# Kernel tuning notes

Hardware: AMD Instinct MI355X
Metric: run time of the kernel (lower is better)

Reference implementation:

```python
import jax, jax.numpy as jnp
import numpy as np

N = 100000
SAMPLE = 25
FEAT = 128
HIDDEN = 128
CLASSES = 40


def setup_inputs() -> dict:
    key = jax.random.key(0)
    k_x, k_n, k_w1, k_w2, k_wl = jax.random.split(key, 5)
    X = jax.random.normal(k_x, (N, FEAT), dtype=jnp.float32)
    neighbors = jax.random.randint(k_n, (N, SAMPLE), 0, N, dtype=jnp.int32)
    # torch Linear weights are [out_features, in_features], xavier-uniform init
    def xavier(k, out_d, in_d):
        bound = float(np.sqrt(6.0 / (in_d + out_d)))
        return jax.random.uniform(k, (out_d, in_d), dtype=jnp.float32, minval=-bound, maxval=bound)
    W1 = xavier(k_w1, HIDDEN, FEAT)
    W2 = xavier(k_w2, HIDDEN, HIDDEN)
    Wlast = xavier(k_wl, CLASSES, HIDDEN)
    return {"X": X, "neighbors": neighbors, "W1": W1, "W2": W2, "Wlast": Wlast}


def reference(X, neighbors, W1, W2, Wlast):
    # forward: for each layer W: X = spmm(adj, X); X = X @ W.T; relu(X)
    # adj row i has sample_num entries of value 1/sample_num -> mean over sampled neighbors
    h = X
    for W in (W1, W2):
        agg = jnp.mean(h[neighbors], axis=1)          # [N, sample, d] -> [N, d]
        h = jax.nn.relu(jnp.einsum('nd,hd->nh', agg, W))
    return jnp.einsum('nh,ch->nc', h, Wlast)          # [N, class_num]
```

## Files before the change

kernel.cpp:

```cpp
#include <hip/hip_runtime.h>
#include <cstdint>
#include <cstddef>

typedef unsigned short u16;
typedef __bf16 bf16x8 __attribute__((ext_vector_type(8)));
typedef u16 u16x8 __attribute__((ext_vector_type(8)));
typedef float f32x4 __attribute__((ext_vector_type(4)));

#define N_NODES 100000
#define SAMPLE 25
#define FEAT 128
#define CLASSES 40

__device__ __forceinline__ float bf2f(u16 v) {
    return __uint_as_float(((unsigned)v) << 16);
}
__device__ __forceinline__ u16 f2bf(float f) {
    unsigned u = __float_as_uint(f);
    u += 0x7FFFu + ((u >> 16) & 1u);
    return (u16)(u >> 16);
}
__device__ __forceinline__ void split_bf(float x, u16& hi, u16& lo) {
    hi = f2bf(x);
    lo = f2bf(x - bf2f(hi));
}

__device__ __forceinline__ void split8(const float* ap, bf16x8& ah, bf16x8& al) {
    union { u16x8 u; bf16x8 b; } H, L;
    #pragma unroll
    for (int j = 0; j < 8; ++j) {
        u16 h, lo; split_bf(ap[j], h, lo);
        H.u[j] = h; L.u[j] = lo;
    }
    ah = H.b; al = L.b;
}

__device__ __forceinline__ f32x4 mfma_split(bf16x8 ah, bf16x8 al,
                                            bf16x8 bh, bf16x8 bl, f32x4 acc) {
    acc = __builtin_amdgcn_mfma_f32_16x16x32_bf16(ah, bh, acc, 0, 0, 0);
    acc = __builtin_amdgcn_mfma_f32_16x16x32_bf16(al, bh, acc, 0, 0, 0);
    acc = __builtin_amdgcn_mfma_f32_16x16x32_bf16(ah, bl, acc, 0, 0, 0);
    return acc;
}

__global__ __launch_bounds__(256) void prep_weights(
    const float* __restrict__ W1, const float* __restrict__ W2,
    const float* __restrict__ Wl,
    u16* __restrict__ w1h, u16* __restrict__ w1l,
    u16* __restrict__ w2h, u16* __restrict__ w2l,
    u16* __restrict__ wlh, u16* __restrict__ wll)
{
    const int i = blockIdx.x * 256 + threadIdx.x;
    const int stride = gridDim.x * 256;
    for (int j = i; j < FEAT * FEAT; j += stride) {
        split_bf(W1[j], w1h[j], w1l[j]);
        split_bf(W2[j], w2h[j], w2l[j]);
    }
    for (int j = i; j < CLASSES * FEAT; j += stride) {
        split_bf(Wl[j], wlh[j], wll[j]);
    }
}

#define NPB32 32

__global__ __launch_bounds__(128) void k1_gemm(
    const float* __restrict__ X,
    const u16* __restrict__ w1h, const u16* __restrict__ w1l,
    u16* __restrict__ Z1)
{
    const int t = threadIdx.x;
    const int w  = t >> 6;
    const int l  = t & 63;
    const int lr = l & 15;
    const int lq = l >> 4;
    const int blockStart = blockIdx.x * NPB32;
    const float* Xrow = X + (size_t)(blockStart + w * 16 + lr) * FEAT;

    bf16x8 ah[4], al[4];
    #pragma unroll
    for (int k = 0; k < 4; ++k) {
        f32x4 x0 = *(const f32x4*)(Xrow + k * 32 + lq * 8);
        f32x4 x1 = *(const f32x4*)(Xrow + k * 32 + lq * 8 + 4);
        float tmp[8];
        #pragma unroll
        for (int j = 0; j < 4; ++j) { tmp[j] = x0[j]; tmp[4 + j] = x1[j]; }
        split8(tmp, ah[k], al[k]);
    }

    #pragma unroll
    for (int c = 0; c < 8; ++c) {
        f32x4 acc = {0.f, 0.f, 0.f, 0.f};
        #pragma unroll
        for (int k = 0; k < 4; ++k) {
            const size_t off = (size_t)(c * 16 + lr) * FEAT + k * 32 + lq * 8;
            bf16x8 bh = *(const bf16x8*)(w1h + off);
            bf16x8 bl = *(const bf16x8*)(w1l + off);
            acc = mfma_split(ah[k], al[k], bh, bl, acc);
        }
        #pragma unroll
        for (int r = 0; r < 4; ++r) {
            int node = blockStart + w * 16 + lq * 4 + r;
            Z1[(size_t)node * FEAT + c * 16 + lr] = f2bf(acc[r]);
        }
    }
}

__global__ __launch_bounds__(128) void k2_hop(
    const u16* __restrict__ Zin, const int* __restrict__ nb,
    const u16* __restrict__ wh, const u16* __restrict__ wl,
    u16* __restrict__ Zout)
{
    __shared__ int nbs[NPB32 * SAMPLE];
    __shared__ float agg[NPB32][FEAT + 4];

    const int t = threadIdx.x;
    const int blockStart = blockIdx.x * NPB32;

    for (int i = t; i < NPB32 * SAMPLE; i += 128)
        nbs[i] = nb[blockStart * SAMPLE + i];
    __syncthreads();

    for (int item = t; item < NPB32 * 16; item += 128) {
        const int nl = item >> 4;
        const int fg = item & 15;
        float acc[8];
        #pragma unroll
        for (int j = 0; j < 8; ++j) acc[j] = 0.f;
        const int* myn = &nbs[nl * SAMPLE];
        #pragma unroll 5
        for (int s = 0; s < SAMPLE; ++s) {
            u16x8 v = *(const u16x8*)(Zin + (size_t)myn[s] * FEAT + fg * 8);
            #pragma unroll
            for (int j = 0; j < 8; ++j) acc[j] += bf2f(v[j]);
        }
        #pragma unroll
        for (int j = 0; j < 8; ++j) {
            float m = acc[j] * (1.0f / SAMPLE);
            agg[nl][fg * 8 + j] = m > 0.f ? m : 0.f;
        }
    }
    __syncthreads();

    const int w  = t >> 6;
    const int l  = t & 63;
    const int lr = l & 15;
    const int lq = l >> 4;

    bf16x8 ah[4], al[4];
    #pragma unroll
    for (int k = 0; k < 4; ++k)
        split8(&agg[w * 16 + lr][k * 32 + lq * 8], ah[k], al[k]);

    #pragma unroll
    for (int c = 0; c < 8; ++c) {
        f32x4 acc = {0.f, 0.f, 0.f, 0.f};
        #pragma unroll
        for (int k = 0; k < 4; ++k) {
            const size_t off = (size_t)(c * 16 + lr) * FEAT + k * 32 + lq * 8;
            bf16x8 bh = *(const bf16x8*)(wh + off);
            bf16x8 bl = *(const bf16x8*)(wl + off);
            acc = mfma_split(ah[k], al[k], bh, bl, acc);
        }
        #pragma unroll
        for (int r = 0; r < 4; ++r) {
            int node = blockStart + w * 16 + lq * 4 + r;
            Zout[(size_t)node * FEAT + c * 16 + lr] = f2bf(acc[r]);
        }
    }
}

__global__ __launch_bounds__(128) void k3_hop(
    const u16* __restrict__ Zin, const int* __restrict__ nb,
    const u16* __restrict__ wh, const u16* __restrict__ wl,
    float* __restrict__ out)
{
    __shared__ int nbs[NPB32 * SAMPLE];
    __shared__ float agg[NPB32][FEAT + 4];

    const int t = threadIdx.x;
    const int blockStart = blockIdx.x * NPB32;

    for (int i = t; i < NPB32 * SAMPLE; i += 128)
        nbs[i] = nb[blockStart * SAMPLE + i];
    __syncthreads();

    for (int item = t; item < NPB32 * 16; item += 128) {
        const int nl = item >> 4;
        const int fg = item & 15;
        float acc[8];
        #pragma unroll
        for (int j = 0; j < 8; ++j) acc[j] = 0.f;
        const int* myn = &nbs[nl * SAMPLE];
        #pragma unroll 5
        for (int s = 0; s < SAMPLE; ++s) {
            u16x8 v = *(const u16x8*)(Zin + (size_t)myn[s] * FEAT + fg * 8);
            #pragma unroll
            for (int j = 0; j < 8; ++j) acc[j] += bf2f(v[j]);
        }
        #pragma unroll
        for (int j = 0; j < 8; ++j) {
            float m = acc[j] * (1.0f / SAMPLE);
            agg[nl][fg * 8 + j] = m > 0.f ? m : 0.f;
        }
    }
    __syncthreads();

    const int w  = t >> 6;
    const int l  = t & 63;
    const int lr = l & 15;
    const int lq = l >> 4;

    bf16x8 ah[4], al[4];
    #pragma unroll
    for (int k = 0; k < 4; ++k)
        split8(&agg[w * 16 + lr][k * 32 + lq * 8], ah[k], al[k]);

    #pragma unroll
    for (int c = 0; c < 3; ++c) {
        const int o = c * 16 + lr;
        f32x4 acc = {0.f, 0.f, 0.f, 0.f};
        #pragma unroll
        for (int k = 0; k < 4; ++k) {
            bf16x8 bh, bl;
            if (o < CLASSES) {
                const size_t off = (size_t)o * FEAT + k * 32 + lq * 8;
                bh = *(const bf16x8*)(wh + off);
                bl = *(const bf16x8*)(wl + off);
            } else {
                #pragma unroll
                for (int j = 0; j < 8; ++j) { bh[j] = (__bf16)0.f; bl[j] = (__bf16)0.f; }
            }
            acc = mfma_split(ah[k], al[k], bh, bl, acc);
        }
        if (o < CLASSES) {
            #pragma unroll
            for (int r = 0; r < 4; ++r) {
                int node = blockStart + w * 16 + lq * 4 + r;
                out[(size_t)node * CLASSES + o] = acc[r];
            }
        }
    }
}

#define NPB 64
#define AGG_STRIDE 136

__global__ __launch_bounds__(256) void gnn_layer1(
    const float* __restrict__ X, const int* __restrict__ nb,
    const u16* __restrict__ w1h, const u16* __restrict__ w1l,
    u16* __restrict__ h1)
{
    __shared__ int nbs[NPB * SAMPLE];
    __shared__ u16 agg_h[NPB][AGG_STRIDE];
    __shared__ u16 agg_l[NPB][AGG_STRIDE];

    const int t = threadIdx.x;
    const int blockStart = blockIdx.x * NPB;

    for (int i = t; i < NPB * SAMPLE; i += 256) {
        int gi = blockStart * SAMPLE + i;
        if (gi >= N_NODES * SAMPLE) gi = N_NODES * SAMPLE - 1;
        nbs[i] = nb[gi];
    }
    __syncthreads();

    for (int item = t; item < NPB * 16; item += 256) {
        const int nl = item >> 4;
        const int fg = item & 15;
        float acc[8];
        #pragma unroll
        for (int j = 0; j < 8; ++j) acc[j] = 0.f;
        const int* myn = &nbs[nl * SAMPLE];
        for (int s = 0; s < SAMPLE; ++s) {
            const float4* p = (const float4*)(X + (size_t)myn[s] * FEAT + fg * 8);
            float4 a = p[0], b = p[1];
            acc[0] += a.x; acc[1] += a.y; acc[2] += a.z; acc[3] += a.w;
            acc[4] += b.x; acc[5] += b.y; acc[6] += b.z; acc[7] += b.w;
        }
        u16x8 oh, ol;
        #pragma unroll
        for (int j = 0; j < 8; ++j) {
            float m = acc[j] * (1.0f / SAMPLE);
            u16 h, lo; split_bf(m, h, lo);
            oh[j] = h; ol[j] = lo;
        }
        *(u16x8*)&agg_h[nl][fg * 8] = oh;
        *(u16x8*)&agg_l[nl][fg * 8] = ol;
    }
    __syncthreads();

    const int w  = t >> 6;
    const int l  = t & 63;
    const int lr = l & 15;
    const int lq = l >> 4;

    bf16x8 ah[4], al[4];
    #pragma unroll
    for (int k = 0; k < 4; ++k) {
        ah[k] = *(const bf16x8*)&agg_h[w * 16 + lr][k * 32 + lq * 8];
        al[k] = *(const bf16x8*)&agg_l[w * 16 + lr][k * 32 + lq * 8];
    }

    #pragma unroll
    for (int c = 0; c < 8; ++c) {
        f32x4 acc = {0.f, 0.f, 0.f, 0.f};
        #pragma unroll
        for (int k = 0; k < 4; ++k) {
            const size_t off = (size_t)(c * 16 + lr) * FEAT + k * 32 + lq * 8;
            bf16x8 bh = *(const bf16x8*)(w1h + off);
            bf16x8 bl = *(const bf16x8*)(w1l + off);
            acc = mfma_split(ah[k], al[k], bh, bl, acc);
        }
        #pragma unroll
        for (int r = 0; r < 4; ++r) {
            int node = blockStart + w * 16 + lq * 4 + r;
            if (node < N_NODES) {
                float v = acc[r] > 0.f ? acc[r] : 0.f;
                h1[(size_t)node * FEAT + c * 16 + lr] = f2bf(v);
            }
        }
    }
}

__global__ __launch_bounds__(256) void gnn_layer2_final(
    const u16* __restrict__ h1, const int* __restrict__ nb,
    const u16* __restrict__ w2h, const u16* __restrict__ w2l,
    const u16* __restrict__ wlh, const u16* __restrict__ wll,
    float* __restrict__ out)
{
    __shared__ int nbs[NPB * SAMPLE];
    __shared__ u16 agg_h[NPB][AGG_STRIDE];
    __shared__ u16 agg_l[NPB][AGG_STRIDE];

    const int t = threadIdx.x;
    const int blockStart = blockIdx.x * NPB;

    for (int i = t; i < NPB * SAMPLE; i += 256) {
        int gi = blockStart * SAMPLE + i;
        if (gi >= N_NODES * SAMPLE) gi = N_NODES * SAMPLE - 1;
        nbs[i] = nb[gi];
    }
    __syncthreads();

    for (int item = t; item < NPB * 16; item += 256) {
        const int nl = item >> 4;
        const int fg = item & 15;
        float acc[8];
        #pragma unroll
        for (int j = 0; j < 8; ++j) acc[j] = 0.f;
        const int* myn = &nbs[nl * SAMPLE];
        for (int s = 0; s < SAMPLE; ++s) {
            u16x8 v = *(const u16x8*)(h1 + (size_t)myn[s] * FEAT + fg * 8);
            #pragma unroll
            for (int j = 0; j < 8; ++j) acc[j] += bf2f(v[j]);
        }
        u16x8 oh, ol;
        #pragma unroll
        for (int j = 0; j < 8; ++j) {
            float m = acc[j] * (1.0f / SAMPLE);
            u16 h, lo; split_bf(m, h, lo);
            oh[j] = h; ol[j] = lo;
        }
        *(u16x8*)&agg_h[nl][fg * 8] = oh;
        *(u16x8*)&agg_l[nl][fg * 8] = ol;
    }
    __syncthreads();

    const int w  = t >> 6;
    const int l  = t & 63;
    const int lr = l & 15;
    const int lq = l >> 4;

    f32x4 hacc[8];
    {
        bf16x8 ah[4], al[4];
        #pragma unroll
        for (int k = 0; k < 4; ++k) {
            ah[k] = *(const bf16x8*)&agg_h[w * 16 + lr][k * 32 + lq * 8];
            al[k] = *(const bf16x8*)&agg_l[w * 16 + lr][k * 32 + lq * 8];
        }
        #pragma unroll
        for (int c = 0; c < 8; ++c) {
            f32x4 acc = {0.f, 0.f, 0.f, 0.f};
            #pragma unroll
            for (int k = 0; k < 4; ++k) {
                const size_t off = (size_t)(c * 16 + lr) * FEAT + k * 32 + lq * 8;
                bf16x8 bh = *(const bf16x8*)(w2h + off);
                bf16x8 bl = *(const bf16x8*)(w2l + off);
                acc = mfma_split(ah[k], al[k], bh, bl, acc);
            }
            hacc[c] = acc;
        }
    }
    __syncthreads();

    #pragma unroll
    for (int c = 0; c < 8; ++c) {
        #pragma unroll
        for (int r = 0; r < 4; ++r) {
            float v = hacc[c][r] > 0.f ? hacc[c][r] : 0.f;
            u16 h, l2; split_bf(v, h, l2);
            agg_h[w * 16 + lq * 4 + r][c * 16 + lr] = h;
            agg_l[w * 16 + lq * 4 + r][c * 16 + lr] = l2;
        }
    }
    __syncthreads();

    {
        bf16x8 ah[4], al[4];
        #pragma unroll
        for (int k = 0; k < 4; ++k) {
            ah[k] = *(const bf16x8*)&agg_h[w * 16 + lr][k * 32 + lq * 8];
            al[k] = *(const bf16x8*)&agg_l[w * 16 + lr][k * 32 + lq * 8];
        }
        #pragma unroll
        for (int c = 0; c < 3; ++c) {
            const int o = c * 16 + lr;
            f32x4 acc = {0.f, 0.f, 0.f, 0.f};
            #pragma unroll
            for (int k = 0; k < 4; ++k) {
                bf16x8 bh, bl;
                if (o < CLASSES) {
                    const size_t off = (size_t)o * FEAT + k * 32 + lq * 8;
                    bh = *(const bf16x8*)(wlh + off);
                    bl = *(const bf16x8*)(wll + off);
                } else {
                    #pragma unroll
                    for (int j = 0; j < 8; ++j) { bh[j] = (__bf16)0.f; bl[j] = (__bf16)0.f; }
                }
                acc = mfma_split(ah[k], al[k], bh, bl, acc);
            }
            if (o < CLASSES) {
                #pragma unroll
                for (int r = 0; r < 4; ++r) {
                    int node = blockStart + w * 16 + lq * 4 + r;
                    if (node < N_NODES) {
                        out[(size_t)node * CLASSES + o] = acc[r];
                    }
                }
            }
        }
    }
}

extern "C" void kernel_launch(void* const* d_in, const int* in_sizes, int n_in,
                              void* d_out, int out_size, void* d_ws, size_t ws_size,
                              hipStream_t stream) {
    const float* X  = (const float*)d_in[0];
    const int*   nb = (const int*)d_in[1];
    const float* W1 = (const float*)d_in[2];
    const float* W2 = (const float*)d_in[3];
    const float* Wl = (const float*)d_in[4];
    float* out = (float*)d_out;

    const size_t zelems = (size_t)N_NODES * FEAT;
    const size_t welems = 4 * (size_t)FEAT * FEAT + 2 * (size_t)CLASSES * FEAT;
    const size_t need_fast = (2 * zelems + welems) * sizeof(u16);

    if (ws_size >= need_fast) {
        u16* Z1  = (u16*)d_ws;
        u16* Z2  = Z1 + zelems;
        u16* w1h = Z2 + zelems;
        u16* w1l = w1h + FEAT * FEAT;
        u16* w2h = w1l + FEAT * FEAT;
        u16* w2l = w2h + FEAT * FEAT;
        u16* wlh = w2l + FEAT * FEAT;
        u16* wll = wlh + CLASSES * FEAT;

        prep_weights<<<64, 256, 0, stream>>>(W1, W2, Wl, w1h, w1l, w2h, w2l, wlh, wll);
        const int blocks = N_NODES / NPB32;
        k1_gemm<<<blocks, 128, 0, stream>>>(X, w1h, w1l, Z1);
        k2_hop<<<blocks, 128, 0, stream>>>(Z1, nb, w2h, w2l, Z2);
        k3_hop<<<blocks, 128, 0, stream>>>(Z2, nb, wlh, wll, out);
    } else {
        u16* h1  = (u16*)d_ws;
        u16* w1h = h1 + zelems;
        u16* w1l = w1h + FEAT * FEAT;
        u16* w2h = w1l + FEAT * FEAT;
        u16* w2l = w2h + FEAT * FEAT;
        u16* wlh = w2l + FEAT * FEAT;
        u16* wll = wlh + CLASSES * FEAT;

        prep_weights<<<64, 256, 0, stream>>>(W1, W2, Wl, w1h, w1l, w2h, w2l, wlh, wll);
        const int blocks = (N_NODES + NPB - 1) / NPB;
        gnn_layer1<<<blocks, 256, 0, stream>>>(X, nb, w1h, w1l, h1);
        gnn_layer2_final<<<blocks, 256, 0, stream>>>(h1, nb, w2h, w2l, wlh, wll, out);
    }
}
```

Measured before the change: 343.1 us.

## Stage GEMM outputs through LDS for coalesced stores and batch neighbor gathers

The k1_gemm and k2_hop epilogues now write MFMA results into an LDS tile and then issue coalesced 16-byte row stores, replacing scattered 2-byte global stores. The gather loops in k2_hop and k3_hop load all 25 neighbor vectors into registers before accumulating, which raises memory-level parallelism. Occupancy hints are added to the launch bounds. In exchange, register pressure rises from the 25-entry buffer, and the LDS staging adds a barrier and reuses the agg buffer.

```diff
diff --git a/kernel.cpp b/kernel.cpp
--- a/kernel.cpp
+++ b/kernel.cpp
@@ -62,12 +62,15 @@
 }
 
 #define NPB32 32
-
-__global__ __launch_bounds__(128) void k1_gemm(
+#define ZT_STRIDE 136
+
+__global__ __launch_bounds__(128, 4) void k1_gemm(
     const float* __restrict__ X,
     const u16* __restrict__ w1h, const u16* __restrict__ w1l,
     u16* __restrict__ Z1)
 {
+    __shared__ u16 zt[NPB32][ZT_STRIDE];
+
     const int t = threadIdx.x;
     const int w  = t >> 6;
     const int l  = t & 63;
@@ -98,20 +101,28 @@
             acc = mfma_split(ah[k], al[k], bh, bl, acc);
         }
         #pragma unroll
-        for (int r = 0; r < 4; ++r) {
-            int node = blockStart + w * 16 + lq * 4 + r;
-            Z1[(size_t)node * FEAT + c * 16 + lr] = f2bf(acc[r]);
-        }
-    }
-}
-
-__global__ __launch_bounds__(128) void k2_hop(
+        for (int r = 0; r < 4; ++r)
+            zt[w * 16 + lq * 4 + r][c * 16 + lr] = f2bf(acc[r]);
+    }
+    __syncthreads();
+
+    #pragma unroll
+    for (int p = 0; p < 4; ++p) {
+        const int idx = p * 128 + t;
+        const int row = idx >> 4;
+        const int col = (idx & 15) * 8;
+        *(u16x8*)(Z1 + (size_t)(blockStart + row) * FEAT + col) =
+            *(const u16x8*)&zt[row][col];
+    }
+}
+
+__global__ __launch_bounds__(128, 3) void k2_hop(
     const u16* __restrict__ Zin, const int* __restrict__ nb,
     const u16* __restrict__ wh, const u16* __restrict__ wl,
     u16* __restrict__ Zout)
 {
     __shared__ int nbs[NPB32 * SAMPLE];
-    __shared__ float agg[NPB32][FEAT + 4];
+    __shared__ float agg[NPB32][132];
 
     const int t = threadIdx.x;
     const int blockStart = blockIdx.x * NPB32;
@@ -120,18 +131,23 @@
         nbs[i] = nb[blockStart * SAMPLE + i];
     __syncthreads();
 
-    for (int item = t; item < NPB32 * 16; item += 128) {
+    #pragma unroll 1
+    for (int it = 0; it < 4; ++it) {
+        const int item = t + it * 128;
         const int nl = item >> 4;
         const int fg = item & 15;
+        const int* myn = &nbs[nl * SAMPLE];
+        u16x8 buf[SAMPLE];
+        #pragma unroll
+        for (int s = 0; s < SAMPLE; ++s)
+            buf[s] = *(const u16x8*)(Zin + ((size_t)myn[s] << 7) + fg * 8);
         float acc[8];
         #pragma unroll
         for (int j = 0; j < 8; ++j) acc[j] = 0.f;
-        const int* myn = &nbs[nl * SAMPLE];
-        #pragma unroll 5
+        #pragma unroll
         for (int s = 0; s < SAMPLE; ++s) {
-            u16x8 v = *(const u16x8*)(Zin + (size_t)myn[s] * FEAT + fg * 8);
             #pragma unroll
-            for (int j = 0; j < 8; ++j) acc[j] += bf2f(v[j]);
+            for (int j = 0; j < 8; ++j) acc[j] += bf2f(buf[s][j]);
         }
         #pragma unroll
         for (int j = 0; j < 8; ++j) {
@@ -150,6 +166,9 @@
     #pragma unroll
     for (int k = 0; k < 4; ++k)
         split8(&agg[w * 16 + lr][k * 32 + lq * 8], ah[k], al[k]);
+    __syncthreads();
+
+    u16* zt = (u16*)agg;
 
     #pragma unroll
     for (int c = 0; c < 8; ++c) {
@@ -162,20 +181,28 @@
             acc = mfma_split(ah[k], al[k], bh, bl, acc);
         }
         #pragma unroll
-        for (int r = 0; r < 4; ++r) {
-            int node = blockStart + w * 16 + lq * 4 + r;
-            Zout[(size_t)node * FEAT + c * 16 + lr] = f2bf(acc[r]);
-        }
-    }
-}
-
-__global__ __launch_bounds__(128) void k3_hop(
+        for (int r = 0; r < 4; ++r)
+            zt[(size_t)(w * 16 + lq * 4 + r) * ZT_STRIDE + c * 16 + lr] = f2bf(acc[r]);
+    }
+    __syncthreads();
+
+    #pragma unroll
+    for (int p = 0; p < 4; ++p) {
+        const int idx = p * 128 + t;
+        const int row = idx >> 4;
+        const int col = (idx & 15) * 8;
+        *(u16x8*)(Zout + (size_t)(blockStart + row) * FEAT + col) =
+            *(const u16x8*)&zt[(size_t)row * ZT_STRIDE + col];
+    }
+}
+
+__global__ __launch_bounds__(128, 3) void k3_hop(
     const u16* __restrict__ Zin, const int* __restrict__ nb,
     const u16* __restrict__ wh, const u16* __restrict__ wl,
     float* __restrict__ out)
 {
     __shared__ int nbs[NPB32 * SAMPLE];
-    __shared__ float agg[NPB32][FEAT + 4];
+    __shared__ float agg[NPB32][132];
 
     const int t = threadIdx.x;
     const int blockStart = blockIdx.x * NPB32;
@@ -184,18 +211,23 @@
         nbs[i] = nb[blockStart * SAMPLE + i];
     __syncthreads();
 
-    for (int item = t; item < NPB32 * 16; item += 128) {
+    #pragma unroll 1
+    for (int it = 0; it < 4; ++it) {
+        const int item = t + it * 128;
         const int nl = item >> 4;
         const int fg = item & 15;
+        const int* myn = &nbs[nl * SAMPLE];
+        u16x8 buf[SAMPLE];
+        #pragma unroll
+        for (int s = 0; s < SAMPLE; ++s)
+            buf[s] = *(const u16x8*)(Zin + ((size_t)myn[s] << 7) + fg * 8);
         float acc[8];
         #pragma unroll
         for (int j = 0; j < 8; ++j) acc[j] = 0.f;
-        const int* myn = &nbs[nl * SAMPLE];
-        #pragma unroll 5
+        #pragma unroll
         for (int s = 0; s < SAMPLE; ++s) {
-            u16x8 v = *(const u16x8*)(Zin + (size_t)myn[s] * FEAT + fg * 8);
             #pragma unroll
-            for (int j = 0; j < 8; ++j) acc[j] += bf2f(v[j]);
+            for (int j = 0; j < 8; ++j) acc[j] += bf2f(buf[s][j]);
         }
         #pragma unroll
         for (int j = 0; j < 8; ++j) {
@@ -235,7 +267,7 @@
         if (o < CLASSES) {
             #pragma unroll
             for (int r = 0; r < 4; ++r) {
-                int node = blockStart + w * 16 + lq * 4 + r;
+                const int node = blockStart + w * 16 + lq * 4 + r;
                 out[(size_t)node * CLASSES + o] = acc[r];
             }
         }
```

New measurement: 328.6 us. 4.2% less time.
